# Kernel optimization log

Hardware: AMD Instinct MI355X
Metric: run time of the kernel (lower is better)

## Reference

```python
import jax, jax.numpy as jnp
import numpy as np

B, S, H = 4, 8192, 1024


def setup_inputs() -> dict:
    key = jax.random.key(0)
    kq, kk, kv, k1, k2, k3, k4 = jax.random.split(key, 7)
    residual_init_factor = 1.0
    return {
        "q": jax.random.normal(kq, (B, S, H), dtype=jnp.float32),
        "k": jax.random.normal(kk, (B, S, H), dtype=jnp.float32),
        "v": jax.random.normal(kv, (B, S, H), dtype=jnp.float32),
        "w_q": 0.01 * jax.random.normal(k1, (H, H), dtype=jnp.float32),
        "w_k": 0.01 * jax.random.normal(k2, (H, H), dtype=jnp.float32),
        "w_v": 0.01 * jax.random.normal(k3, (H, H), dtype=jnp.float32),
        "w_p": 0.01 * residual_init_factor * jax.random.normal(k4, (H, H), dtype=jnp.float32),
    }


def reference(q, k, v, w_q, w_k, w_v, w_p):
    # Projections: [B,S,H] @ [H,H]
    emb_q = jnp.einsum("bsh,hd->bsd", q, w_q)
    emb_k = jnp.einsum("bsh,hd->bsd", k, w_k)
    emb_v = jnp.einsum("bsh,hd->bsd", v, w_v)
    # AFT-simple: per-channel exponential-weighted causal prefix average
    k_exp = jnp.exp(emb_k)
    k_exp_prefix = jnp.cumsum(k_exp, axis=1)
    k_exp_v_prefix = jnp.cumsum(k_exp * emb_v, axis=1)
    y = jax.nn.sigmoid(emb_q) * (k_exp_v_prefix / k_exp_prefix)
    return jnp.einsum("bsh,hd->bsd", y, w_p)
```

## Files before the change

### kernel.cpp

```cpp
#include <hip/hip_runtime.h>
#include <hip/hip_bf16.h>
#include <cstdint>

#define AS_GLOBAL __attribute__((address_space(1)))
#define AS_LDS    __attribute__((address_space(3)))

typedef __attribute__((ext_vector_type(8))) short bf16x8;
typedef __attribute__((ext_vector_type(8))) unsigned short u16x8;
typedef __attribute__((ext_vector_type(4))) float f32x4;

static __device__ __forceinline__ ushort f2bf(float x) {
    union { float f; uint32_t u; } c;
    c.f = x;
    uint32_t u = c.u;
    u += 0x7fffu + ((u >> 16) & 1u);
    return (ushort)(u >> 16);
}
static __device__ __forceinline__ float bf2f(ushort u) {
    union { uint32_t i; float f; } c;
    c.i = ((uint32_t)u) << 16;
    return c.f;
}

static __device__ __forceinline__ void gload_lds16(const void* g, void* l) {
    __builtin_amdgcn_global_load_lds(
        (const AS_GLOBAL uint32_t*)(uintptr_t)g,
        (AS_LDS uint32_t*)(uint32_t)(uintptr_t)l,
        16, 0, 0);
}

__global__ __launch_bounds__(256)
void cvt_f32_bf16(const float4* __restrict__ in, u16x8* __restrict__ out, int n8) {
    int i = blockIdx.x * 256 + threadIdx.x;
    int stride = gridDim.x * 256;
    for (; i < n8; i += stride) {
        float4 a = in[i * 2], b = in[i * 2 + 1];
        u16x8 o;
        o[0] = f2bf(a.x); o[1] = f2bf(a.y); o[2] = f2bf(a.z); o[3] = f2bf(a.w);
        o[4] = f2bf(b.x); o[5] = f2bf(b.y); o[6] = f2bf(b.z); o[7] = f2bf(b.w);
        out[i] = o;
    }
}

__global__ __launch_bounds__(256)
void transpose4_to_bf16(const float* __restrict__ w0, const float* __restrict__ w1,
                        const float* __restrict__ w2, const float* __restrict__ w3,
                        ushort* __restrict__ t0, ushort* __restrict__ t1,
                        ushort* __restrict__ t2, ushort* __restrict__ t3) {
    const int K = 1024, N = 1024;
    __shared__ float tile[32][33];
    const float* w; ushort* wt;
    switch (blockIdx.z) {
        case 0: w = w0; wt = t0; break;
        case 1: w = w1; wt = t1; break;
        case 2: w = w2; wt = t2; break;
        default: w = w3; wt = t3; break;
    }
    int bn = blockIdx.x * 32;
    int bk = blockIdx.y * 32;
    int tx = threadIdx.x & 31, ty = threadIdx.x >> 5;
    #pragma unroll
    for (int i = 0; i < 32; i += 8)
        tile[ty + i][tx] = w[(size_t)(bk + ty + i) * N + bn + tx];
    __syncthreads();
    #pragma unroll
    for (int i = 0; i < 32; i += 8)
        wt[(size_t)(bn + ty + i) * K + bk + tx] = f2bf(tile[tx][ty + i]);
}

template<int EPI, int OUT_BF>
__global__ __launch_bounds__(512, 2)
void gemm8p(const ushort* __restrict__ A, const ushort* __restrict__ Bt,
            void* __restrict__ Cv) {
    constexpr int K = 1024, N = 1024;
    __shared__ alignas(16) ushort sA[2][16384];
    __shared__ alignas(16) ushort sB[2][16384];
    const int tid  = threadIdx.x;
    const int wid  = tid >> 6;
    const int lane = tid & 63;
    const int wr = wid >> 2, wc = wid & 3;
    const int lr = lane & 15;
    const int kb = lane >> 4;
    const int x7 = lr & 7;

    const int wg = blockIdx.x;
    const int xcd = wg & 7, local = wg >> 3;
    const int bm = xcd * 16 + (local >> 2);
    const int bn = local & 3;
    const int m0 = bm * 256, n0 = bn * 256;

    f32x4 acc[8][4] = {};
    bf16x8 af[4][2];
    bf16x8 bv[2][2];

    auto stageA = [&](int tile, int buf, int mh) {
        const int kt0 = tile * 64;
        #pragma unroll
        for (int j = 0; j < 2; j++) {
            int c = j * 512 + tid;
            int rl = c >> 3, p = c & 7;
            int s = p ^ (rl & 7);
            int gr = (rl >> 6) * 128 + mh * 64 + (rl & 63);
            gload_lds16(A + (size_t)(m0 + gr) * K + kt0 + s * 8,
                        &sA[buf][mh * 8192 + c * 8]);
        }
    };
    auto stageB = [&](int tile, int buf, int nh) {
        const int kt0 = tile * 64;
        #pragma unroll
        for (int j = 0; j < 2; j++) {
            int c = j * 512 + tid;
            int cl = c >> 3, p = c & 7;
            int s = p ^ (cl & 7);
            int gc = (cl >> 5) * 64 + nh * 32 + (cl & 31);
            gload_lds16(Bt + (size_t)(n0 + gc) * K + kt0 + s * 8,
                        &sB[buf][nh * 8192 + c * 8]);
        }
    };
    auto readA = [&](int buf, int mq) {
        #pragma unroll
        for (int m = 0; m < 4; m++)
            #pragma unroll
            for (int kh = 0; kh < 2; kh++)
                af[m][kh] = *(const bf16x8*)&sA[buf][mq * 8192
                              + (wr * 64 + m * 16 + lr) * 64
                              + ((kh * 4 + kb) ^ x7) * 8];
    };
    auto readB = [&](int buf, int nq) {
        #pragma unroll
        for (int n = 0; n < 2; n++)
            #pragma unroll
            for (int kh = 0; kh < 2; kh++)
                bv[n][kh] = *(const bf16x8*)&sB[buf][nq * 8192
                              + (wc * 32 + n * 16 + lr) * 64
                              + ((kh * 4 + kb) ^ x7) * 8];
    };
    auto mfma16 = [&](int mq, int nq) {
        #pragma unroll
        for (int m = 0; m < 4; m++)
            #pragma unroll
            for (int n = 0; n < 2; n++) {
                acc[mq*4+m][nq*2+n] = __builtin_amdgcn_mfma_f32_16x16x32_bf16(
                    af[m][0], bv[n][0], acc[mq*4+m][nq*2+n], 0, 0, 0);
                acc[mq*4+m][nq*2+n] = __builtin_amdgcn_mfma_f32_16x16x32_bf16(
                    af[m][1], bv[n][1], acc[mq*4+m][nq*2+n], 0, 0, 0);
            }
    };

#define PHASE(MQ, NQ, READS, STAGES, ENDW) { \
    READS \
    STAGES \
    asm volatile("" ::: "memory"); \
    __builtin_amdgcn_s_barrier(); \
    asm volatile("s_waitcnt lgkmcnt(0)" ::: "memory"); \
    __builtin_amdgcn_s_setprio(1); \
    mfma16(MQ, NQ); \
    __builtin_amdgcn_s_setprio(0); \
    ENDW \
    asm volatile("" ::: "memory"); \
    __builtin_amdgcn_s_barrier(); \
    asm volatile("" ::: "memory"); \
}

    stageA(0, 0, 0); stageA(0, 0, 1); stageB(0, 0, 0); stageB(0, 0, 1);
    stageA(1, 1, 0); stageA(1, 1, 1); stageB(1, 1, 0); stageB(1, 1, 1);
    asm volatile("s_waitcnt vmcnt(0)" ::: "memory");
    __builtin_amdgcn_s_barrier();
    asm volatile("" ::: "memory");

    for (int i = 0; i < 8; i++) {
        const int t = 2 * i;
        const int bt = t & 1, bt1 = bt ^ 1;
        PHASE(0, 0,
            { readA(bt, 0); readB(bt, 0); },
            { if (i > 0) stageA(t + 1, bt1, 0); },
            { asm volatile("s_waitcnt vmcnt(6)" ::: "memory"); })
        PHASE(1, 0,
            { readA(bt, 1); },
            { if (i > 0) stageA(t + 1, bt1, 1); },
            { })
        PHASE(1, 1,
            { readB(bt, 1); },
            { if (i < 7) stageB(t + 2, bt, 0); },
            { })
        PHASE(0, 1,
            { readA(bt, 0); },
            { if (i < 7) stageB(t + 2, bt, 1); },
            { if (i < 7) asm volatile("s_waitcnt vmcnt(6)" ::: "memory");
              else       asm volatile("s_waitcnt vmcnt(0)" ::: "memory"); })
        PHASE(0, 0,
            { readA(bt1, 0); readB(bt1, 0); },
            { if (i < 7) stageA(t + 2, bt, 0); },
            { asm volatile("s_waitcnt vmcnt(6)" ::: "memory"); })
        PHASE(1, 0,
            { readA(bt1, 1); },
            { if (i < 7) stageA(t + 2, bt, 1); },
            { })
        PHASE(1, 1,
            { readB(bt1, 1); },
            { if (i < 7) stageB(t + 3, bt1, 0); },
            { })
        PHASE(0, 1,
            { readA(bt1, 0); },
            { if (i < 7) stageB(t + 3, bt1, 1); },
            { if (i < 7) asm volatile("s_waitcnt vmcnt(6)" ::: "memory"); })
    }
#undef PHASE

    float*  Cf = (float*)Cv;
    ushort* Cb = (ushort*)Cv;
    #pragma unroll
    for (int am = 0; am < 8; am++) {
        #pragma unroll
        for (int an = 0; an < 4; an++) {
            #pragma unroll
            for (int r = 0; r < 4; r++) {
                int row = m0 + wr * 128 + (am >> 2) * 64 + (am & 3) * 16 + (lane >> 4) * 4 + r;
                int col = n0 + wc * 64 + (an >> 1) * 32 + (an & 1) * 16 + lr;
                float v = acc[am][an][r];
                if (EPI == 1) v = 1.0f / (1.0f + __expf(-v));
                else if (EPI == 2) v = __expf(v);
                size_t idx = (size_t)row * N + col;
                if (OUT_BF) Cb[idx] = f2bf(v);
                else        Cf[idx] = v;
            }
        }
    }
}

__global__ __launch_bounds__(256)
void scan_partials(const ushort* __restrict__ ke, const ushort* __restrict__ ev,
                   float* __restrict__ pke, float* __restrict__ pkv) {
    const int H = 1024, S = 8192, CHUNK = 32, BH = 4096;
    int c  = blockIdx.x * 2 + (threadIdx.x >> 7);
    int h0 = (threadIdx.x & 127) * 8;
    int b  = blockIdx.y;
    size_t base = ((size_t)b * S + (size_t)c * CHUNK) * H + h0;
    float se[8] = {}, sv[8] = {};
    for (int s = 0; s < CHUNK; s++) {
        u16x8 e8 = *(const u16x8*)(ke + base + (size_t)s * H);
        u16x8 v8 = *(const u16x8*)(ev + base + (size_t)s * H);
        #pragma unroll
        for (int i = 0; i < 8; i++) {
            float e = bf2f(e8[i]);
            se[i] += e;
            sv[i] += e * bf2f(v8[i]);
        }
    }
    size_t p = (size_t)c * BH + b * H + h0;
    *(float4*)(pke + p)     = make_float4(se[0], se[1], se[2], se[3]);
    *(float4*)(pke + p + 4) = make_float4(se[4], se[5], se[6], se[7]);
    *(float4*)(pkv + p)     = make_float4(sv[0], sv[1], sv[2], sv[3]);
    *(float4*)(pkv + p + 4) = make_float4(sv[4], sv[5], sv[6], sv[7]);
}

__global__ __launch_bounds__(256)
void scan_offsets(float* __restrict__ pke, float* __restrict__ pkv, int nch, int BH) {
    int i = blockIdx.x * blockDim.x + threadIdx.x;
    if (i >= BH) return;
    float rke = 0.f, rkv = 0.f;
    #pragma unroll 8
    for (int c = 0; c < nch; c++) {
        size_t idx = (size_t)c * BH + i;
        float a = pke[idx], b = pkv[idx];
        pke[idx] = rke; pkv[idx] = rkv;
        rke += a; rkv += b;
    }
}

__global__ __launch_bounds__(256)
void scan_final(const ushort* __restrict__ ke, const ushort* __restrict__ ev,
                const ushort* __restrict__ sq,
                const float* __restrict__ pke, const float* __restrict__ pkv,
                ushort* __restrict__ ybf) {
    const int H = 1024, S = 8192, CHUNK = 32, BH = 4096;
    int c  = blockIdx.x * 2 + (threadIdx.x >> 7);
    int h0 = (threadIdx.x & 127) * 8;
    int b  = blockIdx.y;
    size_t p = (size_t)c * BH + b * H + h0;
    float rke[8], rkv[8];
    *(float4*)(rke)     = *(const float4*)(pke + p);
    *(float4*)(rke + 4) = *(const float4*)(pke + p + 4);
    *(float4*)(rkv)     = *(const float4*)(pkv + p);
    *(float4*)(rkv + 4) = *(const float4*)(pkv + p + 4);
    size_t base = ((size_t)b * S + (size_t)c * CHUNK) * H + h0;
    for (int s = 0; s < CHUNK; s++) {
        size_t idx = base + (size_t)s * H;
        u16x8 e8 = *(const u16x8*)(ke + idx);
        u16x8 v8 = *(const u16x8*)(ev + idx);
        u16x8 q8 = *(const u16x8*)(sq + idx);
        u16x8 o;
        #pragma unroll
        for (int i = 0; i < 8; i++) {
            float e = bf2f(e8[i]);
            rke[i] += e;
            rkv[i] += e * bf2f(v8[i]);
            o[i] = f2bf(bf2f(q8[i]) * (rkv[i] / rke[i]));
        }
        *(u16x8*)(ybf + idx) = o;
    }
}

extern "C" void kernel_launch(void* const* d_in, const int* in_sizes, int n_in,
                              void* d_out, int out_size, void* d_ws, size_t ws_size,
                              hipStream_t stream) {
    const float* q   = (const float*)d_in[0];
    const float* k   = (const float*)d_in[1];
    const float* v   = (const float*)d_in[2];
    const float* w_q = (const float*)d_in[3];
    const float* w_k = (const float*)d_in[4];
    const float* w_v = (const float*)d_in[5];
    const float* w_p = (const float*)d_in[6];
    float* out = (float*)d_out;

    const int B = 4, S = 8192, H = 1024;
    const int M = B * S;
    const size_t MH = (size_t)M * H;
    const int NCH = 256;
    const int BH = B * H;

    char* ws = (char*)d_ws;
    size_t off = 0;
    auto alloc = [&](size_t bytes) -> char* {
        char* p = ws + off;
        off += (bytes + 255) & ~(size_t)255;
        return p;
    };
    ushort* abuf = (ushort*)alloc(MH * 2);
    ushort* wqt  = (ushort*)alloc((size_t)H * H * 2);
    ushort* wkt  = (ushort*)alloc((size_t)H * H * 2);
    ushort* wvt  = (ushort*)alloc((size_t)H * H * 2);
    ushort* wpt  = (ushort*)alloc((size_t)H * H * 2);
    ushort* sqb  = (ushort*)alloc(MH * 2);
    ushort* keb  = (ushort*)alloc(MH * 2);
    ushort* evb  = (ushort*)alloc(MH * 2);
    float*  pke  = (float*)alloc((size_t)NCH * BH * 4);
    float*  pkv  = (float*)alloc((size_t)NCH * BH * 4);

    const int ngg = (M / 256) * (H / 256);
    dim3 tg(H / 32, H / 32, 4);
    dim3 gs(NCH / 2, B);
    const int n8 = (int)(MH / 8);

    transpose4_to_bf16<<<tg, 256, 0, stream>>>(w_q, w_k, w_v, w_p, wqt, wkt, wvt, wpt);

    cvt_f32_bf16<<<2048, 256, 0, stream>>>((const float4*)q, (u16x8*)abuf, n8);
    gemm8p<1, 1><<<ngg, 512, 0, stream>>>(abuf, wqt, sqb);
    cvt_f32_bf16<<<2048, 256, 0, stream>>>((const float4*)k, (u16x8*)abuf, n8);
    gemm8p<2, 1><<<ngg, 512, 0, stream>>>(abuf, wkt, keb);
    cvt_f32_bf16<<<2048, 256, 0, stream>>>((const float4*)v, (u16x8*)abuf, n8);
    gemm8p<0, 1><<<ngg, 512, 0, stream>>>(abuf, wvt, evb);

    scan_partials<<<gs, 256, 0, stream>>>(keb, evb, pke, pkv);
    scan_offsets<<<BH / 256, 256, 0, stream>>>(pke, pkv, NCH, BH);
    scan_final<<<gs, 256, 0, stream>>>(keb, evb, sqb, pke, pkv, abuf);

    gemm8p<0, 0><<<ngg, 512, 0, stream>>>(abuf, wpt, out);
}
```

Baseline: 511.3 us.

## Fuse chunk partial sums for the scan into the K and V GEMM epilogues

The per-chunk sums of exp(k) and exp(k)*v are now computed inside the K and V projection GEMM epilogues, using cross-lane shuffles over 32-row groups. This removes the separate scan_partials kernel and its full re-read of both bf16 intermediates. The V GEMM epilogue now reads the exp(k) buffer from global memory, which adds traffic and register pressure inside the epilogue. Partial sums are accumulated from bf16-rounded values so they stay consistent with the final scan.

Result: slower. 588.0 us (+15.0%).

```diff
diff --git a/kernel.cpp b/kernel.cpp
--- a/kernel.cpp
+++ b/kernel.cpp
@@ -68,10 +68,11 @@
         wt[(size_t)(bn + ty + i) * K + bk + tx] = f2bf(tile[tx][ty + i]);
 }
 
-template<int EPI, int OUT_BF>
+template<int EPI, int OUT_BF, int PART>
 __global__ __launch_bounds__(512, 2)
 void gemm8p(const ushort* __restrict__ A, const ushort* __restrict__ Bt,
-            void* __restrict__ Cv) {
+            void* __restrict__ Cv, const ushort* __restrict__ ke_in,
+            float* __restrict__ part_out) {
     constexpr int K = 1024, N = 1024;
     __shared__ alignas(16) ushort sA[2][16384];
     __shared__ alignas(16) ushort sB[2][16384];
@@ -209,49 +210,58 @@
 
     float*  Cf = (float*)Cv;
     ushort* Cb = (ushort*)Cv;
-    #pragma unroll
-    for (int am = 0; am < 8; am++) {
+    if (PART == 0) {
+        #pragma unroll
+        for (int am = 0; am < 8; am++) {
+            #pragma unroll
+            for (int an = 0; an < 4; an++) {
+                #pragma unroll
+                for (int r = 0; r < 4; r++) {
+                    int row = m0 + wr * 128 + (am >> 2) * 64 + (am & 3) * 16 + (lane >> 4) * 4 + r;
+                    int col = n0 + wc * 64 + (an >> 1) * 32 + (an & 1) * 16 + lr;
+                    float v = acc[am][an][r];
+                    if (EPI == 1) v = 1.0f / (1.0f + __expf(-v));
+                    else if (EPI == 2) v = __expf(v);
+                    size_t idx = (size_t)row * N + col;
+                    if (OUT_BF) Cb[idx] = f2bf(v);
+                    else        Cf[idx] = v;
+                }
+            }
+        }
+    } else {
         #pragma unroll
         for (int an = 0; an < 4; an++) {
-            #pragma unroll
-            for (int r = 0; r < 4; r++) {
-                int row = m0 + wr * 128 + (am >> 2) * 64 + (am & 3) * 16 + (lane >> 4) * 4 + r;
-                int col = n0 + wc * 64 + (an >> 1) * 32 + (an & 1) * 16 + lr;
-                float v = acc[am][an][r];
-                if (EPI == 1) v = 1.0f / (1.0f + __expf(-v));
-                else if (EPI == 2) v = __expf(v);
-                size_t idx = (size_t)row * N + col;
-                if (OUT_BF) Cb[idx] = f2bf(v);
-                else        Cf[idx] = v;
+            const int col = n0 + wc * 64 + (an >> 1) * 32 + (an & 1) * 16 + lr;
+            #pragma unroll
+            for (int ap = 0; ap < 4; ap++) {
+                float csum = 0.f;
+                #pragma unroll
+                for (int h = 0; h < 2; h++) {
+                    const int am = ap * 2 + h;
+                    const int rbase = m0 + wr * 128 + (am >> 2) * 64 + (am & 3) * 16 + (lane >> 4) * 4;
+                    #pragma unroll
+                    for (int r = 0; r < 4; r++) {
+                        float v = acc[am][an][r];
+                        if (EPI == 2) v = __expf(v);
+                        ushort vb = f2bf(v);
+                        size_t idx = (size_t)(rbase + r) * N + col;
+                        Cb[idx] = vb;
+                        float vr = bf2f(vb);
+                        if (PART == 1) csum += vr;
+                        else           csum += bf2f(ke_in[idx]) * vr;
+                    }
+                }
+                csum += __shfl_xor(csum, 16, 64);
+                csum += __shfl_xor(csum, 32, 64);
+                if ((lane >> 4) == 0) {
+                    const int row0 = m0 + wr * 128 + ((ap * 2) >> 2) * 64 + ((ap * 2) & 3) * 16;
+                    const int bb = row0 >> 13;
+                    const int cc = (row0 & 8191) >> 5;
+                    part_out[(size_t)cc * 4096 + bb * 1024 + col] = csum;
+                }
             }
         }
     }
-}
-
-__global__ __launch_bounds__(256)
-void scan_partials(const ushort* __restrict__ ke, const ushort* __restrict__ ev,
-                   float* __restrict__ pke, float* __restrict__ pkv) {
-    const int H = 1024, S = 8192, CHUNK = 32, BH = 4096;
-    int c  = blockIdx.x * 2 + (threadIdx.x >> 7);
-    int h0 = (threadIdx.x & 127) * 8;
-    int b  = blockIdx.y;
-    size_t base = ((size_t)b * S + (size_t)c * CHUNK) * H + h0;
-    float se[8] = {}, sv[8] = {};
-    for (int s = 0; s < CHUNK; s++) {
-        u16x8 e8 = *(const u16x8*)(ke + base + (size_t)s * H);
-        u16x8 v8 = *(const u16x8*)(ev + base + (size_t)s * H);
-        #pragma unroll
-        for (int i = 0; i < 8; i++) {
-            float e = bf2f(e8[i]);
-            se[i] += e;
-            sv[i] += e * bf2f(v8[i]);
-        }
-    }
-    size_t p = (size_t)c * BH + b * H + h0;
-    *(float4*)(pke + p)     = make_float4(se[0], se[1], se[2], se[3]);
-    *(float4*)(pke + p + 4) = make_float4(se[4], se[5], se[6], se[7]);
-    *(float4*)(pkv + p)     = make_float4(sv[0], sv[1], sv[2], sv[3]);
-    *(float4*)(pkv + p + 4) = make_float4(sv[4], sv[5], sv[6], sv[7]);
 }
 
 __global__ __launch_bounds__(256)
@@ -345,15 +355,14 @@
     transpose4_to_bf16<<<tg, 256, 0, stream>>>(w_q, w_k, w_v, w_p, wqt, wkt, wvt, wpt);
 
     cvt_f32_bf16<<<2048, 256, 0, stream>>>((const float4*)q, (u16x8*)abuf, n8);
-    gemm8p<1, 1><<<ngg, 512, 0, stream>>>(abuf, wqt, sqb);
+    gemm8p<1, 1, 0><<<ngg, 512, 0, stream>>>(abuf, wqt, sqb, nullptr, nullptr);
     cvt_f32_bf16<<<2048, 256, 0, stream>>>((const float4*)k, (u16x8*)abuf, n8);
-    gemm8p<2, 1><<<ngg, 512, 0, stream>>>(abuf, wkt, keb);
+    gemm8p<2, 1, 1><<<ngg, 512, 0, stream>>>(abuf, wkt, keb, nullptr, pke);
     cvt_f32_bf16<<<2048, 256, 0, stream>>>((const float4*)v, (u16x8*)abuf, n8);
-    gemm8p<0, 1><<<ngg, 512, 0, stream>>>(abuf, wvt, evb);
-
-    scan_partials<<<gs, 256, 0, stream>>>(keb, evb, pke, pkv);
+    gemm8p<0, 1, 2><<<ngg, 512, 0, stream>>>(abuf, wvt, evb, keb, pkv);
+
     scan_offsets<<<BH / 256, 256, 0, stream>>>(pke, pkv, NCH, BH);
     scan_final<<<gs, 256, 0, stream>>>(keb, evb, sqb, pke, pkv, abuf);
 
-    gemm8p<0, 0><<<ngg, 512, 0, stream>>>(abuf, wpt, out);
-}
+    gemm8p<0, 0, 0><<<ngg, 512, 0, stream>>>(abuf, wpt, out, nullptr, nullptr);
+}
```
